# Optimization experiments

Hardware: AMD Instinct MI355X
Metric: run time of the kernel (lower is better)

The kernel has to match this reference:

```python
import jax, jax.numpy as jnp
import numpy as np

# 3x3 Hessian/derivative stencils (match torch tensors in edge_mask_deptehwise)
_DII = jnp.array([[0., 1., 0.], [0., -2., 0.], [0., 1., 0.]], jnp.float32).reshape(1, 1, 3, 3)
_DIJ = 0.25 * jnp.array([[1., 0., -1.], [0., 0., 0.], [-1., 0., 1.]], jnp.float32).reshape(1, 1, 3, 3)
_DJJ = jnp.array([[0., 0., 0.], [1., -2., 1.], [0., 0., 0.]], jnp.float32).reshape(1, 1, 3, 3)


def _conv3x3(x, kern):  # x: [1,1,h,w], zero padding 1 (matches F.conv2d padding=1)
    return jax.lax.conv_general_dilated(x, kern, (1, 1), ((1, 1), (1, 1)))


def _edge_mask(x, edge_thld):  # x: [1,1,h,w] -> bool [1,1,h,w]
    dii = _conv3x3(x, _DII)
    dij = _conv3x3(x, _DIJ)
    djj = _conv3x3(x, _DJJ)
    det = dii * djj - dij * dij
    tr = dii + djj
    thld = (edge_thld + 1) ** 2 / edge_thld
    return (tr * tr / det <= thld) & (det > 0)


def _max_pool(x, ksize):  # stride 1, padding 1 (matches F.max_pool2d(..., padding=1))
    return jax.lax.reduce_window(x, -jnp.inf, jax.lax.max,
                                 (1, 1, ksize, ksize), (1, 1, 1, 1),
                                 ((0, 0), (0, 0), (1, 1), (1, 1)))


def setup_inputs() -> dict:
    key = jax.random.key(0)
    k1, k2 = jax.random.split(key)
    h = w = 4096
    score_map = jax.random.uniform(k1, (1, 1, h, w), dtype=jnp.float32)
    valid_depth_mask = jax.random.randint(k2, (h, w), 0, 2).astype(jnp.bool_)
    return {
        'score_map': score_map,
        'valid_depth_mask': valid_depth_mask,
        'k': 4096,
        'score_thld': 0,
        'edge_thld': 10,
        'nms_size': 3,
        'eof_size': 5,
    }


def reference(score_map, valid_depth_mask, k, score_thld, edge_thld, nms_size, eof_size):
    b, c, h, w = score_map.shape  # b = c = 1 (extract_kpts reshapes to (h, w))
    mask = score_map > score_thld
    if nms_size > 0:
        nms_max = _max_pool(score_map, nms_size)
        mask = (score_map == nms_max) & mask
    if eof_size > 0:
        ri = jnp.arange(h)
        cj = jnp.arange(w)
        eof = ((ri >= eof_size) & (ri < h - eof_size))[:, None] & \
              ((cj >= eof_size) & (cj < w - eof_size))[None, :]
        mask = eof[None, None] & mask
    if edge_thld > 0:
        mask = _edge_mask(score_map, edge_thld) & mask
    mask2d = mask.reshape(h, w) & valid_depth_mask
    flat_scores = score_map.reshape(h * w)
    # nonzero + argsort(desc)[:k] + gather  ==  top_k over -inf-masked scores
    masked = jnp.where(mask2d.reshape(-1), flat_scores, -jnp.inf)
    _, idx = jax.lax.top_k(masked, k)
    rows = idx // w
    cols = idx % w
    indices = jnp.stack([rows, cols], axis=0)[None]  # [1, 2, k]
    scores = flat_scores[idx][None]                  # [1, k]
    return indices, scores
```

## Files before the change

### kernel.cpp

```cpp
#include <hip/hip_runtime.h>
#include <stdint.h>

#define H 4096
#define W 4096
#define EOFS 5
#define K_TOP 4096
#define NB 65536
#define SLOT_CAP 8192
#define RPB 8
#define NRG 511
#define NCG 4
#define NBLK (NRG * NCG)
#define CBUF 512
#define EMIT_LDS (K_TOP + 128)


__device__ __forceinline__ unsigned int bucket_of(float s) {
    float u = s * s;
    float u2 = u * u;
    float u4 = u2 * u2;
    float s9 = u4 * s;
    unsigned int b = (unsigned int)(s9 * 65536.0f);
    return b > 65535u ? 65535u : b;
}

__global__ void zero_kernel(unsigned int* hist, unsigned int* pivot,
                            unsigned int* candCount) {
    int p = blockIdx.x * blockDim.x + threadIdx.x;
    if (p < NB) hist[p] = 0u;
    if (p == 0) { pivot[0] = 0u; candCount[0] = 0u; }
}

#define LOADROW6(arr, p)                                                       \
    {                                                                          \
        const float* _p = (p);                                                 \
        arr[0] = _p[-1];                                                       \
        float4 _q = *(const float4*)_p;                                        \
        arr[1] = _q.x; arr[2] = _q.y; arr[3] = _q.z; arr[4] = _q.w;            \
        arr[5] = _p[4];                                                        \
    }

__global__ __launch_bounds__(256)
void collect_kernel(const float* __restrict__ x, const int* __restrict__ vmask,
                    unsigned int* __restrict__ hist,
                    unsigned long long* __restrict__ cand,
                    unsigned int* __restrict__ candCount,
                    unsigned int cand_cap, int do_cand) {
    __shared__ unsigned long long buf[CBUF];
    __shared__ unsigned int cnt, gbase;
    int t = threadIdx.x;
    if (t == 0) cnt = 0u;
    __syncthreads();

    int rowgroup = (int)blockIdx.x >> 2;
    int cg = (int)blockIdx.x & 3;
    int j0 = cg * 1024 + t * 4;
    bool active = !((cg == 0 && t == 0) || (cg == NCG - 1 && t == 255));
    int r0 = EOFS + rowgroup * RPB;
    int rend = r0 + RPB - 1;
    if (rend > H - 1 - EOFS) rend = H - 1 - EOFS;

    float A[6], B[6], C[6], vm[6];
    if (active) {
        LOADROW6(A, x + (size_t)(r0 - 1) * W + j0);
        LOADROW6(B, x + (size_t)r0 * W + j0);
    }
    for (int i = r0; i <= rend; ++i) {
        if (active) {
            LOADROW6(C, x + (size_t)(i + 1) * W + j0);
            #pragma unroll
            for (int c = 0; c < 6; ++c)
                vm[c] = fmaxf(fmaxf(A[c], B[c]), C[c]);
            #pragma unroll
            for (int k = 1; k <= 4; ++k) {
                int j = j0 + k - 1;
                if (j >= EOFS && j <= W - 1 - EOFS) {
                    float e = B[k];
                    if (e > 0.0f) {
                        float m = fmaxf(fmaxf(vm[k - 1], vm[k]), vm[k + 1]);
                        if (e >= m) {
                            float dii = (A[k] - 2.0f * e) + C[k];
                            float djj = (B[k - 1] - 2.0f * e) + B[k + 1];
                            float dij = 0.25f * (((A[k - 1] - A[k + 1]) - C[k - 1]) + C[k + 1]);
                            float det = dii * djj - dij * dij;
                            if (det > 0.0f) {
                                float tr = dii + djj;
                                if (tr * tr / det <= 12.1f) {
                                    if (vmask[(size_t)i * W + j] != 0) {
                                        unsigned int pos = atomicAdd(&cnt, 1u);
                                        if (pos < CBUF) {
                                            atomicAdd(&hist[bucket_of(e)], 1u);
                                            unsigned int fb = __float_as_uint(e);
                                            unsigned int idx =
                                                (unsigned int)i * W + (unsigned int)j;
                                            buf[pos] =
                                                ((unsigned long long)fb << 32) |
                                                (unsigned int)(~idx);
                                        }
                                    }
                                }
                            }
                        }
                    }
                }
            }
            #pragma unroll
            for (int c = 0; c < 6; ++c) { A[c] = B[c]; B[c] = C[c]; }
        }
    }

    __syncthreads();
    if (do_cand) {
        unsigned int c = cnt;
        if (c > CBUF) c = CBUF;
        if (t == 0) gbase = atomicAdd(candCount, c);
        __syncthreads();
        unsigned int g0 = gbase;
        for (unsigned int p = t; p < c; p += 256)
            if (g0 + p < cand_cap) cand[g0 + p] = buf[p];
    }
}

__global__ __launch_bounds__(64)
void coarse_kernel(const unsigned int* __restrict__ hist,
                   unsigned int* __restrict__ coarse) {
    int c = blockIdx.x, t = threadIdx.x;
    const unsigned int* h = hist + c * 256;
    unsigned int s = h[t] + h[t + 64] + h[t + 128] + h[t + 192];
    for (int off = 32; off > 0; off >>= 1) s += __shfl_down(s, off, 64);
    if (t == 0) coarse[c] = s;
}

__global__ __launch_bounds__(256)
void chunkscan_kernel(const unsigned int* __restrict__ coarse,
                      unsigned int* __restrict__ chunkExcl) {
    __shared__ unsigned int s[256];
    int t = threadIdx.x;
    unsigned int mine = coarse[t];
    s[t] = mine;
    __syncthreads();
    for (int off = 1; off < 256; off <<= 1) {
        unsigned int v = (t + off < 256) ? s[t + off] : 0u;
        __syncthreads();
        s[t] += v;
        __syncthreads();
    }
    chunkExcl[t] = s[t] - mine;
}

__global__ __launch_bounds__(256)
void basefill_kernel(const unsigned int* __restrict__ hist,
                     const unsigned int* __restrict__ chunkExcl,
                     unsigned int* __restrict__ base,
                     unsigned int* __restrict__ pivotOut) {
    __shared__ unsigned int s[256];
    int t = threadIdx.x;
    int b = blockIdx.x * 256 + t;
    unsigned int h = hist[b];
    s[t] = h;
    __syncthreads();
    for (int off = 1; off < 256; off <<= 1) {
        unsigned int v = (t + off < 256) ? s[t + off] : 0u;
        __syncthreads();
        s[t] += v;
        __syncthreads();
    }
    unsigned int bb = chunkExcl[blockIdx.x] + s[t] - h;
    base[b] = bb;
    if (bb < (unsigned int)K_TOP && bb + h >= (unsigned int)K_TOP)
        pivotOut[0] = (unsigned int)b;
}

__global__ __launch_bounds__(256)
void scatter_cand_kernel(const unsigned long long* __restrict__ cand,
                         const unsigned int* __restrict__ candCount,
                         const unsigned int* __restrict__ pivotPtr,
                         unsigned int* __restrict__ base,
                         unsigned long long* __restrict__ slots,
                         unsigned int cand_cap) {
    unsigned int n = *candCount;
    if (n > cand_cap) n = cand_cap;
    unsigned int pivot = *pivotPtr;
    unsigned int stride = gridDim.x * blockDim.x;
    for (unsigned int p = blockIdx.x * blockDim.x + threadIdx.x; p < n; p += stride) {
        unsigned long long k = cand[p];
        unsigned int fb = (unsigned int)(k >> 32);
        unsigned int bkt = bucket_of(__uint_as_float(fb));
        if (bkt >= pivot) {
            unsigned int pos = atomicAdd(&base[bkt], 1u);
            if (pos < (unsigned int)SLOT_CAP) slots[pos] = k;
        }
    }
}

__global__ void scatter_full_kernel(const float* __restrict__ x,
                                    const int* __restrict__ vmask,
                                    const unsigned int* __restrict__ pivotPtr,
                                    unsigned int* __restrict__ base,
                                    unsigned long long* __restrict__ slots) {
    int j = EOFS + blockIdx.x * blockDim.x + threadIdx.x;
    int i = EOFS + blockIdx.y;
    if (j > W - 1 - EOFS) return;
    const float* r0p = x + (size_t)(i - 1) * W + j;
    const float* r1p = x + (size_t)i * W + j;
    const float* r2p = x + (size_t)(i + 1) * W + j;
    float a = r0p[-1], b = r0p[0], c = r0p[1];
    float d = r1p[-1], e = r1p[0], f = r1p[1];
    float g = r2p[-1], h2 = r2p[0], i2 = r2p[1];
    if (!(e > 0.0f)) return;
    float m = fmaxf(fmaxf(fmaxf(a, b), fmaxf(c, d)),
                    fmaxf(fmaxf(f, g), fmaxf(h2, i2)));
    if (!(e >= m)) return;
    float dii = (b - 2.0f * e) + h2;
    float djj = (d - 2.0f * e) + f;
    float dij = 0.25f * (((a - c) - g) + i2);
    float det = dii * djj - dij * dij;
    if (!(det > 0.0f)) return;
    float tr = dii + djj;
    if (!(tr * tr / det <= 12.1f)) return;
    if (vmask[(size_t)i * W + j] == 0) return;
    unsigned int bkt = bucket_of(e);
    if (bkt >= pivotPtr[0]) {
        unsigned int pos = atomicAdd(&base[bkt], 1u);
        if (pos < (unsigned int)SLOT_CAP) {
            unsigned int idx = (unsigned int)i * W + (unsigned int)j;
            slots[pos] = ((unsigned long long)__float_as_uint(e) << 32)
                       | (unsigned int)(~idx);
        }
    }
}

__global__ __launch_bounds__(1024, 1)
void emit_kernel(const unsigned int* __restrict__ baseAfter,
                 const unsigned int* __restrict__ pivotPtr,
                 const unsigned long long* __restrict__ slots,
                 float* __restrict__ out) {
    __shared__ unsigned long long lds[EMIT_LDS];
    int t = threadIdx.x;
    for (int p = t; p < EMIT_LDS; p += 1024) lds[p] = slots[p];
    __syncthreads();
    unsigned int pivot = pivotPtr[0];
    for (int b = (int)pivot + t; b < NB; b += 1024) {
        unsigned int start = (b == 65535) ? 0u : baseAfter[b + 1];
        unsigned int end = baseAfter[b];
        if (end > (unsigned int)SLOT_CAP) end = (unsigned int)SLOT_CAP;
        if (end <= start || start >= (unsigned int)K_TOP) continue;
        unsigned int len = end - start;
        if (len > 128u) len = 128u;
        if (start + len > (unsigned int)EMIT_LDS) len = (unsigned int)EMIT_LDS - start;
        unsigned long long* a = &lds[start];
        for (unsigned int r = 1; r < len; ++r) {
            unsigned long long key = a[r];
            int q = (int)r - 1;
            while (q >= 0 && a[q] < key) { a[q + 1] = a[q]; --q; }
            a[q + 1] = key;
        }
        unsigned int emitN = len;
        if (start + emitN > (unsigned int)K_TOP) emitN = (unsigned int)K_TOP - start;
        for (unsigned int r = 0; r < emitN; ++r) {
            unsigned long long key = a[r];
            unsigned int fb = (unsigned int)(key >> 32);
            unsigned int idx = ~((unsigned int)key);
            unsigned int rank = start + r;
            out[rank]             = (float)(idx >> 12);
            out[K_TOP + rank]     = (float)(idx & (W - 1));
            out[2 * K_TOP + rank] = __uint_as_float(fb);
        }
    }
}

extern "C" void kernel_launch(void* const* d_in, const int* in_sizes, int n_in,
                              void* d_out, int out_size, void* d_ws, size_t ws_size,
                              hipStream_t stream) {
    const float* score = (const float*)d_in[0];
    const int* vmask = (const int*)d_in[1];
    unsigned char* ws = (unsigned char*)d_ws;
    unsigned int* hist      = (unsigned int*)ws;
    unsigned int* base      = (unsigned int*)(ws + 262144);
    unsigned int* coarse    = (unsigned int*)(ws + 524288);
    unsigned int* chunkExcl = (unsigned int*)(ws + 525312);
    unsigned int* pivot     = (unsigned int*)(ws + 526336);
    unsigned int* candCount = (unsigned int*)(ws + 526340);
    unsigned long long* slots = (unsigned long long*)(ws + 526848);
    unsigned long long* cand  = (unsigned long long*)(ws + 655360);
    float* out = (float*)d_out;

    unsigned int cand_cap = 0;
    int do_cand = 0;
    if (ws_size >= 655360ull + 8ull * 1000000ull) {
        size_t cap = (ws_size - 655360ull) / 8ull;
        if (cap > 2097152ull) cap = 2097152ull;
        cand_cap = (unsigned int)cap;
        do_cand = 1;
    }

    zero_kernel<<<(NB + 255) / 256, 256, 0, stream>>>(hist, pivot, candCount);

    collect_kernel<<<NBLK, 256, 0, stream>>>(score, vmask, hist, cand,
                                             candCount, cand_cap, do_cand);
    coarse_kernel<<<256, 64, 0, stream>>>(hist, coarse);
    chunkscan_kernel<<<1, 256, 0, stream>>>(coarse, chunkExcl);
    basefill_kernel<<<256, 256, 0, stream>>>(hist, chunkExcl, base, pivot);

    if (do_cand) {
        scatter_cand_kernel<<<512, 256, 0, stream>>>(cand, candCount, pivot,
                                                     base, slots, cand_cap);
    } else {
        dim3 blk(256, 1, 1), grd(16, H - 2 * EOFS, 1);
        scatter_full_kernel<<<grd, blk, 0, stream>>>(score, vmask, pivot, base, slots);
    }
    emit_kernel<<<1, 1024, 0, stream>>>(base, pivot, slots, out);
}
```

Before: 238.8 us.

## Merge histogram scan kernels into one early-exit pivot scan; batch histogram atomics

Replaces the three-kernel coarse/chunk/base prefix-scan pipeline with a single 1024-thread block. It scans the histogram from the top buckets downward and stops once the running count reaches K, which removes two launches and most of the histogram reads. The global histogram atomics also move out of the inner stencil loop into a post-pass over each block's LDS candidate buffer, which shortens the divergent hot path. The trade-off is a serial single-block scan. Base entries below the pivot chunk are left unwritten, which is fine if later kernels only read buckets at or above the pivot.

```diff
diff --git a/kernel.cpp b/kernel.cpp
--- a/kernel.cpp
+++ b/kernel.cpp
@@ -89,7 +89,6 @@
                                     if (vmask[(size_t)i * W + j] != 0) {
                                         unsigned int pos = atomicAdd(&cnt, 1u);
                                         if (pos < CBUF) {
-                                            atomicAdd(&hist[bucket_of(e)], 1u);
                                             unsigned int fb = __float_as_uint(e);
                                             unsigned int idx =
                                                 (unsigned int)i * W + (unsigned int)j;
@@ -110,9 +109,14 @@
     }
 
     __syncthreads();
+    unsigned int c = cnt;
+    if (c > CBUF) c = CBUF;
+    for (unsigned int p = t; p < c; p += 256) {
+        unsigned long long k = buf[p];
+        float s = __uint_as_float((unsigned int)(k >> 32));
+        atomicAdd(&hist[bucket_of(s)], 1u);
+    }
     if (do_cand) {
-        unsigned int c = cnt;
-        if (c > CBUF) c = CBUF;
         if (t == 0) gbase = atomicAdd(candCount, c);
         __syncthreads();
         unsigned int g0 = gbase;
@@ -121,54 +125,36 @@
     }
 }
 
-__global__ __launch_bounds__(64)
-void coarse_kernel(const unsigned int* __restrict__ hist,
-                   unsigned int* __restrict__ coarse) {
-    int c = blockIdx.x, t = threadIdx.x;
-    const unsigned int* h = hist + c * 256;
-    unsigned int s = h[t] + h[t + 64] + h[t + 128] + h[t + 192];
-    for (int off = 32; off > 0; off >>= 1) s += __shfl_down(s, off, 64);
-    if (t == 0) coarse[c] = s;
-}
-
-__global__ __launch_bounds__(256)
-void chunkscan_kernel(const unsigned int* __restrict__ coarse,
-                      unsigned int* __restrict__ chunkExcl) {
-    __shared__ unsigned int s[256];
+__global__ __launch_bounds__(1024)
+void pivotbase_kernel(const unsigned int* __restrict__ hist,
+                      unsigned int* __restrict__ base,
+                      unsigned int* __restrict__ pivotOut) {
+    __shared__ unsigned int s[1024];
+    __shared__ unsigned int carry_s;
     int t = threadIdx.x;
-    unsigned int mine = coarse[t];
-    s[t] = mine;
-    __syncthreads();
-    for (int off = 1; off < 256; off <<= 1) {
-        unsigned int v = (t + off < 256) ? s[t + off] : 0u;
-        __syncthreads();
-        s[t] += v;
-        __syncthreads();
-    }
-    chunkExcl[t] = s[t] - mine;
-}
-
-__global__ __launch_bounds__(256)
-void basefill_kernel(const unsigned int* __restrict__ hist,
-                     const unsigned int* __restrict__ chunkExcl,
-                     unsigned int* __restrict__ base,
-                     unsigned int* __restrict__ pivotOut) {
-    __shared__ unsigned int s[256];
-    int t = threadIdx.x;
-    int b = blockIdx.x * 256 + t;
-    unsigned int h = hist[b];
-    s[t] = h;
-    __syncthreads();
-    for (int off = 1; off < 256; off <<= 1) {
-        unsigned int v = (t + off < 256) ? s[t + off] : 0u;
-        __syncthreads();
-        s[t] += v;
-        __syncthreads();
-    }
-    unsigned int bb = chunkExcl[blockIdx.x] + s[t] - h;
-    base[b] = bb;
-    if (bb < (unsigned int)K_TOP && bb + h >= (unsigned int)K_TOP)
-        pivotOut[0] = (unsigned int)b;
+    if (t == 0) carry_s = 0u;
+    __syncthreads();
+    for (int chunk = NB - 1024; chunk >= 0; chunk -= 1024) {
+        unsigned int carry = carry_s;
+        unsigned int h = hist[chunk + t];
+        s[t] = h;
+        __syncthreads();
+        for (int off = 1; off < 1024; off <<= 1) {
+            unsigned int v = (t + off < 1024) ? s[t + off] : 0u;
+            __syncthreads();
+            s[t] += v;
+            __syncthreads();
+        }
+        unsigned int bb = carry + s[t] - h;
+        base[chunk + t] = bb;
+        if (bb < (unsigned int)K_TOP && bb + h >= (unsigned int)K_TOP)
+            pivotOut[0] = (unsigned int)(chunk + t);
+        unsigned int total = s[0];
+        __syncthreads();
+        if (t == 0) carry_s = carry + total;
+        __syncthreads();
+        if (carry + total >= (unsigned int)K_TOP) break;
+    }
 }
 
 __global__ __launch_bounds__(256)
@@ -277,8 +263,6 @@
     unsigned char* ws = (unsigned char*)d_ws;
     unsigned int* hist      = (unsigned int*)ws;
     unsigned int* base      = (unsigned int*)(ws + 262144);
-    unsigned int* coarse    = (unsigned int*)(ws + 524288);
-    unsigned int* chunkExcl = (unsigned int*)(ws + 525312);
     unsigned int* pivot     = (unsigned int*)(ws + 526336);
     unsigned int* candCount = (unsigned int*)(ws + 526340);
     unsigned long long* slots = (unsigned long long*)(ws + 526848);
@@ -298,9 +282,7 @@
 
     collect_kernel<<<NBLK, 256, 0, stream>>>(score, vmask, hist, cand,
                                              candCount, cand_cap, do_cand);
-    coarse_kernel<<<256, 64, 0, stream>>>(hist, coarse);
-    chunkscan_kernel<<<1, 256, 0, stream>>>(coarse, chunkExcl);
-    basefill_kernel<<<256, 256, 0, stream>>>(hist, chunkExcl, base, pivot);
+    pivotbase_kernel<<<1, 1024, 0, stream>>>(hist, base, pivot);
 
     if (do_cand) {
         scatter_cand_kernel<<<512, 256, 0, stream>>>(cand, candCount, pivot,
```

After: 249.0 us. 4.2% more time.
